# Optimization experiments

Measured on AMD Instinct MI355X. Metric: run time of the kernel, lower is better.

The kernel has to match this reference:

```python
import jax, jax.numpy as jnp
import numpy as np

H = 16            # num heads (sharded)
NOPE = 128        # qk_nope_head_dim
ROPE = 64         # qk_rope_head_dim
VD = 128          # v_head_dim
KV_RANK = 512
HEAD = NOPE + ROPE  # 192
SCALE = HEAD ** (-0.5)  # mscale == 1 (no yarn scaling)
EPS = 1e-6


def rmsnorm(x, w):
    var = jnp.mean(x * x, axis=-1, keepdims=True)
    return x * jax.lax.rsqrt(var + EPS) * w


def apply_rope(pe, cos, sin):
    # pe: [T, h, ROPE]; torch code de-interleaves pairs then applies
    # non-interleaved (rotate-half) rope: out = [e*cos - o*sin, o*cos + e*sin]
    e = pe[..., 0::2]
    o = pe[..., 1::2]
    c = cos[:, None, :]
    s = sin[:, None, :]
    return jnp.concatenate([e * c - o * s, o * c + e * s], axis=-1)


def setup_inputs() -> dict:
    key = jax.random.key(0)
    ks = jax.random.split(key, 10)
    T, D = 4096, 2048
    w = 0.02
    return {
        "hidden_states": jax.random.normal(ks[0], (T, D), jnp.float32),
        "cos": jax.random.uniform(ks[1], (T, ROPE // 2), jnp.float32),
        "sin": jax.random.uniform(ks[2], (T, ROPE // 2), jnp.float32),
        "w_q_a": jax.random.normal(ks[3], (D, 1536), jnp.float32) * w,
        "q_a_ln_w": jnp.ones((1536,), jnp.float32),
        "w_q_b": jax.random.normal(ks[4], (1536, H * HEAD), jnp.float32) * w,
        "w_kv_a": jax.random.normal(ks[5], (D, KV_RANK + ROPE), jnp.float32) * w,
        "kv_a_ln_w": jnp.ones((KV_RANK,), jnp.float32),
        "w_kv_b": jax.random.normal(ks[6], (KV_RANK, H * (NOPE + VD)), jnp.float32) * w,
        "w_o": jax.random.normal(ks[7], (H * VD, D), jnp.float32) * w,
        "batch_size": 2,
    }


def reference(hidden_states, cos, sin, w_q_a, q_a_ln_w, w_q_b, w_kv_a,
              kv_a_ln_w, w_kv_b, w_o, batch_size):
    T, D = hidden_states.shape
    B = int(batch_size)
    S = T // B

    # Q: low-rank down proj -> RMSNorm -> up proj
    q = rmsnorm(hidden_states @ w_q_a, q_a_ln_w) @ w_q_b
    q = q.reshape(T, H, HEAD)
    q_nope = q[..., :NOPE]
    q_pe = apply_rope(q[..., NOPE:], cos, sin)

    # KV: joint down proj with shared rope part (MQA-style)
    ckv = hidden_states @ w_kv_a                        # [T, 512+64]
    compressed_kv = ckv[:, :KV_RANK]
    k_pe = apply_rope(ckv[:, KV_RANK:][:, None, :], cos, sin)  # [T, 1, 64]
    kv = (rmsnorm(compressed_kv, kv_a_ln_w) @ w_kv_b).reshape(T, H, NOPE + VD)
    k_nope = kv[..., :NOPE]
    v = kv[..., NOPE:]                                   # [T, H, 128]

    # Assemble full query/key heads (value pad to 192 + final slice is a no-op
    # mathematically since padded dims are zero; we keep value dim = 128).
    query = jnp.concatenate([q_nope, q_pe], axis=-1)     # [T, H, 192]
    key = jnp.concatenate([k_nope, jnp.broadcast_to(k_pe, (T, H, ROPE))], axis=-1)

    # Causal (prefill) attention per sequence
    qb = query.reshape(B, S, H, HEAD)
    kb = key.reshape(B, S, H, HEAD)
    vb = v.reshape(B, S, H, VD)
    scores = jnp.einsum("bqhd,bkhd->bhqk", qb, kb) * SCALE
    causal = jnp.tril(jnp.ones((S, S), bool))
    scores = jnp.where(causal, scores, jnp.finfo(scores.dtype).min)
    probs = jax.nn.softmax(scores, axis=-1)
    attn = jnp.einsum("bhqk,bkhd->bqhd", probs, vb)      # [B, S, H, 128]

    return attn.reshape(T, H * VD) @ w_o
```

## Files before the change

### kernel.cpp

```cpp
#include <hip/hip_runtime.h>
#include <cstdint>
#include <cstddef>

#define TT 4096
#define DD 2048
#define NH 16
#define HEADD 192
#define NOPE 128
#define VDIM 128
#define SEQ 2048

typedef __bf16 bf16x8 __attribute__((ext_vector_type(8)));
typedef float f32x4 __attribute__((ext_vector_type(4)));
typedef unsigned int u32;

__device__ __forceinline__ float bf2f(unsigned short u) {
    union { unsigned int i; float f; } v; v.i = ((unsigned int)u) << 16; return v.f;
}
__device__ __forceinline__ unsigned short f2bf(float f) {
    union { float f; unsigned int i; } v; v.f = f;
    unsigned int r = v.i + 0x7FFFu + ((v.i >> 16) & 1u);
    return (unsigned short)(r >> 16);
}
__device__ __forceinline__ u32 pack2bf(float a, float b) {
    return (u32)f2bf(a) | ((u32)f2bf(b) << 16);
}
__device__ __forceinline__ void gload16(const unsigned short* g, unsigned short* l) {
    __builtin_amdgcn_global_load_lds((const __attribute__((address_space(1))) u32*)g,
                                     (__attribute__((address_space(3))) u32*)l, 16, 0, 0);
}

#define GMFMA __builtin_amdgcn_mfma_f32_16x16x32_bf16

__global__ __launch_bounds__(256) void cvt_bf16_k(const float* __restrict__ x,
                                                  unsigned short* __restrict__ y, int n) {
    int i = (blockIdx.x * 256 + threadIdx.x) * 4;
    if (i < n) {
        float4 v = *(const float4*)(x + i);
        uint2 o;
        o.x = pack2bf(v.x, v.y);
        o.y = pack2bf(v.z, v.w);
        *(uint2*)(y + i) = o;
    }
}

__global__ __launch_bounds__(256) void transpose_cvt_k(const float* __restrict__ W,
                                                       unsigned short* __restrict__ Wt,
                                                       int K, int N) {
    __shared__ float tile[32][33];
    int n0 = blockIdx.x * 32, k0 = blockIdx.y * 32;
    int t = threadIdx.x, lr = t >> 5, lc = t & 31;
#pragma unroll
    for (int p = 0; p < 4; p++) {
        int k = k0 + lr + p * 8, n = n0 + lc;
        tile[lr + p * 8][lc] = (k < K && n < N) ? W[(size_t)k * N + n] : 0.f;
    }
    __syncthreads();
#pragma unroll
    for (int p = 0; p < 4; p++) {
        int n = n0 + lr + p * 8, k = k0 + lc;
        if (n < N && k < K) Wt[(size_t)n * K + k] = f2bf(tile[lc][lr + p * 8]);
    }
}

template <int BN, typename OT>
__global__ __launch_bounds__(512) void gemm256_k(const unsigned short* __restrict__ A,
                                                 const unsigned short* __restrict__ Bt,
                                                 OT* __restrict__ C,
                                                 int M, int N, int K) {
    constexpr int NREP = BN / 64;
    constexpr int NB = BN / 64;
    constexpr int TILE_E = 8192 + BN * 64;
    __shared__ __align__(16) unsigned short lds[2 * TILE_E];
    const int t = threadIdx.x;
    const int w = t >> 6, lane = t & 63;
    const int wr = w >> 2, wc = w & 3;
    const int l15 = lane & 15, quad = lane >> 4;
    const int bm = blockIdx.y * 128, bn = blockIdx.x * BN;
    const int srow = w * 8 + (lane >> 3);
    const int scol = 8 * ((lane & 7) ^ (lane >> 3));
    const unsigned short* Ag = A + (size_t)(bm + srow) * K + scol;
    const unsigned short* Bg = Bt + (size_t)(bn + srow) * K + scol;
    const int rc0 = (quad * 8) ^ ((l15 & 7) * 8);
    const int rc1 = (32 + quad * 8) ^ ((l15 & 7) * 8);
    f32x4 acc[4][NREP];
    f32x4 zero = {0.f, 0.f, 0.f, 0.f};
#pragma unroll
    for (int i = 0; i < 4; i++)
#pragma unroll
        for (int n = 0; n < NREP; n++) acc[i][n] = zero;
    const int NT = K >> 6;
#pragma unroll
    for (int c = 0; c < 2; c++)
        gload16(Ag + (size_t)c * 64 * K, &lds[c * 4096 + w * 512]);
#pragma unroll
    for (int c = 0; c < NB; c++)
        gload16(Bg + (size_t)c * 64 * K, &lds[8192 + c * 4096 + w * 512]);

    for (int kt = 0; kt < NT; kt++) {
        const int cb = (kt & 1) * TILE_E;
        const int nb = TILE_E - cb;
        const bool more = (kt + 1) < NT;
        asm volatile("s_waitcnt vmcnt(0)" ::: "memory");
        __builtin_amdgcn_s_barrier();
        asm volatile("" ::: "memory");
        const unsigned short* Agk = Ag + (size_t)(kt + 1) * 64;
        const unsigned short* Bgk = Bg + (size_t)(kt + 1) * 64;
        if (more) {
            gload16(Agk, &lds[nb + w * 512]);
            gload16(Agk + (size_t)64 * K, &lds[nb + 4096 + w * 512]);
#pragma unroll
            for (int c = 0; c < NB / 2; c++)
                gload16(Bgk + (size_t)c * 64 * K, &lds[nb + 8192 + c * 4096 + w * 512]);
        }
        bf16x8 a0[2][2], b[NREP][2];
#pragma unroll
        for (int j = 0; j < 2; j++) {
            int rl = wr * 64 + j * 16 + l15;
            a0[j][0] = *(const bf16x8*)&lds[cb + rl * 64 + rc0];
            a0[j][1] = *(const bf16x8*)&lds[cb + rl * 64 + rc1];
        }
#pragma unroll
        for (int n = 0; n < NREP; n++) {
            int rl = wc * (BN / 4) + n * 16 + l15;
            b[n][0] = *(const bf16x8*)&lds[cb + 8192 + rl * 64 + rc0];
            b[n][1] = *(const bf16x8*)&lds[cb + 8192 + rl * 64 + rc1];
        }
        __builtin_amdgcn_s_setprio(1);
#pragma unroll
        for (int j = 0; j < 2; j++)
#pragma unroll
            for (int n = 0; n < NREP; n++) {
                acc[j][n] = GMFMA(a0[j][0], b[n][0], acc[j][n], 0, 0, 0);
                acc[j][n] = GMFMA(a0[j][1], b[n][1], acc[j][n], 0, 0, 0);
            }
        __builtin_amdgcn_s_setprio(0);
        __builtin_amdgcn_s_barrier();
        if (more) {
#pragma unroll
            for (int c = NB / 2; c < NB; c++)
                gload16(Bgk + (size_t)c * 64 * K, &lds[nb + 8192 + c * 4096 + w * 512]);
        }
        bf16x8 a1[2][2];
#pragma unroll
        for (int j = 0; j < 2; j++) {
            int rl = wr * 64 + 32 + j * 16 + l15;
            a1[j][0] = *(const bf16x8*)&lds[cb + rl * 64 + rc0];
            a1[j][1] = *(const bf16x8*)&lds[cb + rl * 64 + rc1];
        }
        __builtin_amdgcn_s_setprio(1);
#pragma unroll
        for (int j = 0; j < 2; j++)
#pragma unroll
            for (int n = 0; n < NREP; n++) {
                acc[2 + j][n] = GMFMA(a1[j][0], b[n][0], acc[2 + j][n], 0, 0, 0);
                acc[2 + j][n] = GMFMA(a1[j][1], b[n][1], acc[2 + j][n], 0, 0, 0);
            }
        __builtin_amdgcn_s_setprio(0);
    }
#pragma unroll
    for (int mi = 0; mi < 4; mi++) {
        int row = bm + wr * 64 + mi * 16 + quad * 4;
#pragma unroll
        for (int n = 0; n < NREP; n++) {
            int col = bn + wc * (BN / 4) + n * 16 + l15;
            OT* cp = C + (size_t)row * N + col;
#pragma unroll
            for (int r = 0; r < 4; r++) {
                float v = acc[mi][n][r];
                if constexpr (sizeof(OT) == 2) cp[(size_t)r * N] = f2bf(v);
                else                            cp[(size_t)r * N] = v;
            }
        }
    }
}

__global__ __launch_bounds__(512) void gemm192_rope_k(const unsigned short* __restrict__ A,
                                                      const unsigned short* __restrict__ Bt,
                                                      const float* __restrict__ cosb,
                                                      const float* __restrict__ sinb,
                                                      unsigned short* __restrict__ Qb) {
    constexpr int K = 1536, N = 3072;
    constexpr int NREP = 3, NB = 3;
    constexpr int TILE_E = 8192 + 192 * 64;
    __shared__ __align__(16) unsigned short lds[2 * TILE_E];
    const int t = threadIdx.x;
    const int w = t >> 6, lane = t & 63;
    const int wr = w >> 2, wc = w & 3;
    const int l15 = lane & 15, quad = lane >> 4;
    const int bm = blockIdx.y * 128, bn = blockIdx.x * 192;
    const int srow = w * 8 + (lane >> 3);
    const int scol = 8 * ((lane & 7) ^ (lane >> 3));
    const unsigned short* Ag = A + (size_t)(bm + srow) * K + scol;
    const unsigned short* Bg = Bt + (size_t)(bn + srow) * K + scol;
    const int rc0 = (quad * 8) ^ ((l15 & 7) * 8);
    const int rc1 = (32 + quad * 8) ^ ((l15 & 7) * 8);
    f32x4 acc[4][NREP];
    f32x4 zero = {0.f, 0.f, 0.f, 0.f};
#pragma unroll
    for (int i = 0; i < 4; i++)
#pragma unroll
        for (int n = 0; n < NREP; n++) acc[i][n] = zero;
    const int NT = K >> 6;
#pragma unroll
    for (int c = 0; c < 2; c++)
        gload16(Ag + (size_t)c * 64 * K, &lds[c * 4096 + w * 512]);
#pragma unroll
    for (int c = 0; c < NB; c++)
        gload16(Bg + (size_t)c * 64 * K, &lds[8192 + c * 4096 + w * 512]);

    for (int kt = 0; kt < NT; kt++) {
        const int cb = (kt & 1) * TILE_E;
        const int nb = TILE_E - cb;
        const bool more = (kt + 1) < NT;
        asm volatile("s_waitcnt vmcnt(0)" ::: "memory");
        __builtin_amdgcn_s_barrier();
        asm volatile("" ::: "memory");
        const unsigned short* Agk = Ag + (size_t)(kt + 1) * 64;
        const unsigned short* Bgk = Bg + (size_t)(kt + 1) * 64;
        if (more) {
            gload16(Agk, &lds[nb + w * 512]);
            gload16(Agk + (size_t)64 * K, &lds[nb + 4096 + w * 512]);
            gload16(Bgk, &lds[nb + 8192 + w * 512]);
        }
        bf16x8 a0[2][2], b[NREP][2];
#pragma unroll
        for (int j = 0; j < 2; j++) {
            int rl = wr * 64 + j * 16 + l15;
            a0[j][0] = *(const bf16x8*)&lds[cb + rl * 64 + rc0];
            a0[j][1] = *(const bf16x8*)&lds[cb + rl * 64 + rc1];
        }
#pragma unroll
        for (int n = 0; n < NREP; n++) {
            int rl = wc * 48 + n * 16 + l15;
            b[n][0] = *(const bf16x8*)&lds[cb + 8192 + rl * 64 + rc0];
            b[n][1] = *(const bf16x8*)&lds[cb + 8192 + rl * 64 + rc1];
        }
        __builtin_amdgcn_s_setprio(1);
#pragma unroll
        for (int j = 0; j < 2; j++)
#pragma unroll
            for (int n = 0; n < NREP; n++) {
                acc[j][n] = GMFMA(a0[j][0], b[n][0], acc[j][n], 0, 0, 0);
                acc[j][n] = GMFMA(a0[j][1], b[n][1], acc[j][n], 0, 0, 0);
            }
        __builtin_amdgcn_s_setprio(0);
        __builtin_amdgcn_s_barrier();
        if (more) {
#pragma unroll
            for (int c = 1; c < NB; c++)
                gload16(Bgk + (size_t)c * 64 * K, &lds[nb + 8192 + c * 4096 + w * 512]);
        }
        bf16x8 a1[2][2];
#pragma unroll
        for (int j = 0; j < 2; j++) {
            int rl = wr * 64 + 32 + j * 16 + l15;
            a1[j][0] = *(const bf16x8*)&lds[cb + rl * 64 + rc0];
            a1[j][1] = *(const bf16x8*)&lds[cb + rl * 64 + rc1];
        }
        __builtin_amdgcn_s_setprio(1);
#pragma unroll
        for (int j = 0; j < 2; j++)
#pragma unroll
            for (int n = 0; n < NREP; n++) {
                acc[2 + j][n] = GMFMA(a1[j][0], b[n][0], acc[2 + j][n], 0, 0, 0);
                acc[2 + j][n] = GMFMA(a1[j][1], b[n][1], acc[2 + j][n], 0, 0, 0);
            }
        __builtin_amdgcn_s_setprio(0);
    }
    __syncthreads();
    unsigned short* Ct = lds;
#pragma unroll
    for (int mi = 0; mi < 4; mi++) {
        int rl = wr * 64 + mi * 16 + quad * 4;
#pragma unroll
        for (int n = 0; n < NREP; n++) {
            int cl = wc * 48 + n * 16 + l15;
#pragma unroll
            for (int r = 0; r < 4; r++)
                Ct[(rl + r) * 200 + cl] = f2bf(acc[mi][n][r]);
        }
    }
    __syncthreads();
    {
        int r = t >> 2, cg = t & 3;
        int trow = bm + r;
        int h = blockIdx.x;
        const float* cr = cosb + (size_t)trow * 32;
        const float* sn = sinb + (size_t)trow * 32;
        unsigned short* dst = Qb + ((size_t)trow * NH + h) * HEADD + cg * 48;
        __align__(16) unsigned short tmp[48];
        const unsigned short* rowp = &Ct[r * 200];
        if (cg < 2) {
#pragma unroll
            for (int i = 0; i < 48; i++) tmp[i] = rowp[cg * 48 + i];
        } else if (cg == 2) {
#pragma unroll
            for (int i = 0; i < 32; i++) tmp[i] = rowp[96 + i];
            const unsigned short* pe = rowp + 128;
#pragma unroll
            for (int jj = 0; jj < 16; jj++) {
                float e = bf2f(pe[2 * jj]), o = bf2f(pe[2 * jj + 1]);
                tmp[32 + jj] = f2bf(e * cr[jj] - o * sn[jj]);
            }
        } else {
            const unsigned short* pe = rowp + 128;
#pragma unroll
            for (int jj = 16; jj < 32; jj++) {
                float e = bf2f(pe[2 * jj]), o = bf2f(pe[2 * jj + 1]);
                tmp[jj - 16] = f2bf(e * cr[jj] - o * sn[jj]);
            }
#pragma unroll
            for (int jj = 0; jj < 32; jj++) {
                float e = bf2f(pe[2 * jj]), o = bf2f(pe[2 * jj + 1]);
                tmp[16 + jj] = f2bf(o * cr[jj] + e * sn[jj]);
            }
        }
#pragma unroll
        for (int g = 0; g < 6; g++)
            *(uint4*)(dst + g * 8) = *(const uint4*)(&tmp[g * 8]);
    }
}

#define KS_STRIDE 200
#define VT_STRIDE 72
#define CS_STRIDE 132

__global__ __launch_bounds__(256) void gemm_kv_k(const unsigned short* __restrict__ A,
                                                 const unsigned short* __restrict__ Bt,
                                                 const unsigned short* __restrict__ kpe,
                                                 unsigned short* __restrict__ Kb2,
                                                 unsigned short* __restrict__ Vt2) {
    const int K = 512;
    __shared__ __align__(16) unsigned short smem[128 * CS_STRIDE];
    unsigned short* As = smem;
    unsigned short* Bs = smem + 128 * 32;
    unsigned short* Cs = smem;
    int bm = blockIdx.y * 128, bn = blockIdx.x * 128;
    int t = threadIdx.x;
    int wave = t >> 6, lane = t & 63;
    int wr = (wave >> 1) * 64, wc = (wave & 1) * 64;
    int l15 = lane & 15, quad = lane >> 4;
    f32x4 acc[4][4];
    f32x4 zero = {0.f, 0.f, 0.f, 0.f};
#pragma unroll
    for (int i = 0; i < 4; i++)
#pragma unroll
        for (int j = 0; j < 4; j++) acc[i][j] = zero;
    int r0 = 16 * (2 * wave) + (lane >> 2);
    int cOff = (lane & 3) * 8;
    const unsigned short* gA0 = A + (size_t)(bm + r0) * K + cOff;
    const unsigned short* gA1 = A + (size_t)(bm + r0 + 16) * K + cOff;
    const unsigned short* gB0 = Bt + (size_t)(bn + r0) * K + cOff;
    const unsigned short* gB1 = Bt + (size_t)(bn + r0 + 16) * K + cOff;
    unsigned short* lA0 = &As[(2 * wave) * 512];
    unsigned short* lA1 = &As[(2 * wave + 1) * 512];
    unsigned short* lB0 = &Bs[(2 * wave) * 512];
    unsigned short* lB1 = &Bs[(2 * wave + 1) * 512];
    for (int k0 = 0; k0 < K; k0 += 32) {
        gload16(gA0 + k0, lA0);
        gload16(gA1 + k0, lA1);
        gload16(gB0 + k0, lB0);
        gload16(gB1 + k0, lB1);
        __syncthreads();
        bf16x8 af[4], bfr[4];
#pragma unroll
        for (int i = 0; i < 4; i++)
            af[i] = *(const bf16x8*)&As[(wr + i * 16 + l15) * 32 + quad * 8];
#pragma unroll
        for (int j = 0; j < 4; j++)
            bfr[j] = *(const bf16x8*)&Bs[(wc + j * 16 + l15) * 32 + quad * 8];
#pragma unroll
        for (int i = 0; i < 4; i++)
#pragma unroll
            for (int j = 0; j < 4; j++)
                acc[i][j] = GMFMA(af[i], bfr[j], acc[i][j], 0, 0, 0);
        __syncthreads();
    }
#pragma unroll
    for (int i = 0; i < 4; i++) {
        int lr = wr + i * 16 + quad * 4;
#pragma unroll
        for (int j = 0; j < 4; j++) {
            int lc = wc + j * 16 + l15;
#pragma unroll
            for (int r = 0; r < 4; r++)
                Cs[(lr + r) * CS_STRIDE + lc] = f2bf(acc[i][j][r]);
        }
    }
    __syncthreads();
    int hh = bn >> 8;
    bool isV = (bn & 255) != 0;
    if (!isV) {
        int row = t >> 1, halfc = t & 1;
        int gs = bm + row;
        int b2 = gs >> 11, s2 = gs & 2047;
        unsigned short* dpb = Kb2 +
            ((size_t)((b2 * NH + hh) * 32 + (s2 >> 6)) * 64 + (s2 & 63)) * KS_STRIDE;
        const unsigned short* sp = &Cs[row * CS_STRIDE + halfc * 64];
        unsigned short* dp = dpb + halfc * 64;
#pragma unroll
        for (int g = 0; g < 8; g++)
            *(uint4*)(dp + g * 8) = *(const uint4*)(sp + g * 8);
        if (halfc) {
            const unsigned short* kp = kpe + (size_t)gs * 64;
            unsigned short* dq = dpb + 128;
#pragma unroll
            for (int g = 0; g < 8; g++)
                *(uint4*)(dq + g * 8) = *(const uint4*)(kp + g * 8);
        }
    } else {
        int kth = t >> 7, dim = t & 127;
        int gs0 = bm + kth * 64;
        int b2 = gs0 >> 11, s20 = gs0 & 2047;
        unsigned short* dp = Vt2 +
            ((size_t)((b2 * NH + hh) * 32 + (s20 >> 6)) * 128 + dim) * VT_STRIDE;
#pragma unroll
        for (int g = 0; g < 8; g++) {
            uint4 o;
            unsigned short* op = (unsigned short*)&o;
#pragma unroll
            for (int q2 = 0; q2 < 8; q2++)
                op[q2] = Cs[(kth * 64 + g * 8 + q2) * CS_STRIDE + dim];
            *(uint4*)(dp + g * 8) = o;
        }
    }
}

__global__ __launch_bounds__(256) void norms_k(const unsigned short* __restrict__ qab,
                                               const float* __restrict__ qw,
                                               const float* __restrict__ kw,
                                               const float* __restrict__ cosb,
                                               const float* __restrict__ sinb,
                                               unsigned short* __restrict__ qan,
                                               unsigned short* __restrict__ ckvn,
                                               unsigned short* __restrict__ kpe) {
    const float QSCALE = 0.07216878364870323f;
    int row = blockIdx.x, t = threadIdx.x;
    const unsigned short* xr = qab + (size_t)row * 2304;
    float s1 = 0.f, s2 = 0.f;
    for (int i = t; i < 1536; i += 256) { float v = bf2f(xr[i]); s1 += v * v; }
#pragma unroll
    for (int i = t; i < 512; i += 256) { float v = bf2f(xr[1536 + i]); s2 += v * v; }
    __shared__ float r1[256], r2[256];
    r1[t] = s1; r2[t] = s2; __syncthreads();
    for (int o = 128; o > 0; o >>= 1) {
        if (t < o) { r1[t] += r1[t + o]; r2[t] += r2[t + o]; }
        __syncthreads();
    }
    float sc1 = rsqrtf(r1[0] / 1536.f + 1e-6f) * QSCALE;
    float sc2 = rsqrtf(r2[0] / 512.f + 1e-6f);
    unsigned short* y1 = qan + (size_t)row * 1536;
    for (int i = t; i < 1536; i += 256) y1[i] = f2bf(bf2f(xr[i]) * sc1 * qw[i]);
    unsigned short* y2 = ckvn + (size_t)row * 512;
#pragma unroll
    for (int i = t; i < 512; i += 256) y2[i] = f2bf(bf2f(xr[1536 + i]) * sc2 * kw[i]);
    if (t < 32) {
        float e = bf2f(xr[2048 + 2 * t]), o = bf2f(xr[2048 + 2 * t + 1]);
        float c = cosb[row * 32 + t], sn = sinb[row * 32 + t];
        kpe[row * 64 + t]      = f2bf(e * c - o * sn);
        kpe[row * 64 + 32 + t] = f2bf(o * c + e * sn);
    }
}

__global__ __launch_bounds__(512) void attn_mfma_k(const unsigned short* __restrict__ Qb,
                                                   const unsigned short* __restrict__ Kb2,
                                                   const unsigned short* __restrict__ Vt2,
                                                   unsigned short* __restrict__ Opart,
                                                   float* __restrict__ Mbuf,
                                                   float* __restrict__ Lbuf) {
    __shared__ __align__(16) unsigned short Ks[64 * KS_STRIDE];
    __shared__ __align__(16) unsigned short Vts[128 * VT_STRIDE];
    int xe = 39 - blockIdx.x;
    int h  = blockIdx.y;
    int b  = blockIdx.z;
    int qt = 0, accn = 0;
    while (true) { int c = (qt >> 2) + 1; if (xe < accn + c) break; accn += c; qt++; }
    int chunk = xe - accn;
    int t = threadIdx.x;
    int w = t >> 6, lane = t & 63;
    int l15 = lane & 15, quad = lane >> 4;
    int bh = b * NH + h;
    int q0 = b * SEQ + qt * 128;
    int qglob = qt * 128 + w * 16 + l15;
    int flat = bh * 40 + xe;

    bf16x8 qf[6];
    {
        const unsigned short* qbase = Qb + ((size_t)(q0 + w * 16 + l15) * NH + h) * HEADD + quad * 8;
#pragma unroll
        for (int c = 0; c < 6; c++)
            qf[c] = *(const bf16x8*)(qbase + c * 32);
    }
    f32x4 acc_o[8];
    f32x4 zero = {0.f, 0.f, 0.f, 0.f};
#pragma unroll
    for (int j = 0; j < 8; j++) acc_o[j] = zero;
    float mrun = -1e30f, lrun = 0.f;

    int kt0 = chunk * 8, kt1 = min(kt0 + 7, 2 * qt + 1);
    int cbeg = w * 5 + min(w, 3), cnt = (w < 3) ? 6 : 5;
    for (int kt = kt0; kt <= kt1; kt++) {
        __syncthreads();
        {
            const unsigned short* kg = Kb2 + ((size_t)bh * 32 + kt) * (64 * KS_STRIDE) + lane * 8;
            const unsigned short* vg = Vt2 + ((size_t)bh * 32 + kt) * (128 * VT_STRIDE) + lane * 8;
            for (int c = cbeg; c < cbeg + cnt; c++) {
                if (c < 25) gload16(kg + c * 512, &Ks[c * 512]);
                else        gload16(vg + (c - 25) * 512, &Vts[(c - 25) * 512]);
            }
        }
        __syncthreads();
        f32x4 acc_s[4];
#pragma unroll
        for (int j = 0; j < 4; j++) acc_s[j] = zero;
#pragma unroll
        for (int c = 0; c < 6; c++) {
#pragma unroll
            for (int j = 0; j < 4; j++) {
                bf16x8 kf = *(const bf16x8*)&Ks[(j * 16 + l15) * KS_STRIDE + c * 32 + quad * 8];
                acc_s[j] = GMFMA(kf, qf[c], acc_s[j], 0, 0, 0);
            }
        }
        float sv[4][4];
        const bool needmask = (kt * 64 + 63) > (qt * 128 + w * 16);
        if (needmask) {
#pragma unroll
            for (int j = 0; j < 4; j++) {
                int kbase = kt * 64 + j * 16 + quad * 4;
#pragma unroll
                for (int r = 0; r < 4; r++)
                    sv[j][r] = (kbase + r > qglob) ? -1e30f : acc_s[j][r];
            }
        } else {
#pragma unroll
            for (int j = 0; j < 4; j++)
#pragma unroll
                for (int r = 0; r < 4; r++) sv[j][r] = acc_s[j][r];
        }
        float v = sv[0][0];
#pragma unroll
        for (int j = 0; j < 4; j++)
#pragma unroll
            for (int r = 0; r < 4; r++) v = fmaxf(v, sv[j][r]);
        v = fmaxf(v, __shfl_xor(v, 16));
        v = fmaxf(v, __shfl_xor(v, 32));
        if (!__all(v - mrun <= 8.f)) {
            float mnew = fmaxf(mrun, v);
            float alpha = __expf(mrun - mnew);
            mrun = mnew;
            lrun *= alpha;
#pragma unroll
            for (int jt = 0; jt < 8; jt++)
#pragma unroll
                for (int r = 0; r < 4; r++) acc_o[jt][r] *= alpha;
        }
        float rs = 0.f;
#pragma unroll
        for (int j = 0; j < 4; j++)
#pragma unroll
            for (int r = 0; r < 4; r++) { float p = __expf(sv[j][r] - mrun); sv[j][r] = p; rs += p; }
        rs += __shfl_xor(rs, 16);
        rs += __shfl_xor(rs, 32);
        lrun += rs;
        u32 pk[4][2];
#pragma unroll
        for (int j = 0; j < 4; j++) {
            pk[j][0] = pack2bf(sv[j][0], sv[j][1]);
            pk[j][1] = pack2bf(sv[j][2], sv[j][3]);
        }
        int laneA = (((2 * quad) & 3) << 4) + l15;
        int laneB = (((2 * quad + 1) & 3) << 4) + l15;
        bool hi = (quad & 2) != 0;
#pragma unroll
        for (int c2 = 0; c2 < 2; c2++) {
            u32 a0 = __shfl(pk[2 * c2][0], laneA),     a1 = __shfl(pk[2 * c2][1], laneA);
            u32 b0 = __shfl(pk[2 * c2 + 1][0], laneA), b1 = __shfl(pk[2 * c2 + 1][1], laneA);
            u32 a2 = __shfl(pk[2 * c2][0], laneB),     a3 = __shfl(pk[2 * c2][1], laneB);
            u32 b2 = __shfl(pk[2 * c2 + 1][0], laneB), b3 = __shfl(pk[2 * c2 + 1][1], laneB);
            union { u32 d[4]; bf16x8 v8; } pf;
            pf.d[0] = hi ? b0 : a0;
            pf.d[1] = hi ? b1 : a1;
            pf.d[2] = hi ? b2 : a2;
            pf.d[3] = hi ? b3 : a3;
#pragma unroll
            for (int jt = 0; jt < 8; jt++) {
                bf16x8 vf = *(const bf16x8*)&Vts[(jt * 16 + l15) * VT_STRIDE + c2 * 32 + quad * 8];
                acc_o[jt] = GMFMA(vf, pf.v8, acc_o[jt], 0, 0, 0);
            }
        }
    }
    {
        int row = w * 16 + l15;
        unsigned short* op = Opart + (size_t)flat * 16384 + row * 128;
#pragma unroll
        for (int jt = 0; jt < 8; jt++) {
            uint2 o;
            o.x = pack2bf(acc_o[jt][0], acc_o[jt][1]);
            o.y = pack2bf(acc_o[jt][2], acc_o[jt][3]);
            *(uint2*)(op + jt * 16 + quad * 4) = o;
        }
        if (quad == 0) {
            Mbuf[(size_t)flat * 128 + row] = mrun;
            Lbuf[(size_t)flat * 128 + row] = lrun;
        }
    }
}

__global__ __launch_bounds__(256) void attn_combine_k(const unsigned short* __restrict__ Opart,
                                                      const float* __restrict__ Mbuf,
                                                      const float* __restrict__ Lbuf,
                                                      unsigned short* __restrict__ attnb) {
    int q64 = blockIdx.x, h = blockIdx.y, b = blockIdx.z;
    int qt = q64 >> 1, half = q64 & 1;
    int nch = (qt >> 2) + 1;
    int F = 0;
    for (int q = 0; q < qt; q++) F += (q >> 2) + 1;
    int flat0 = (b * NH + h) * 40 + F;
    int t = threadIdx.x;
    int row = t >> 2, d0 = (t & 3) * 32;
    int row128 = half * 64 + row;
    float mc[4], lc[4], wgt[4];
    float mstar = -1e30f;
#pragma unroll
    for (int c = 0; c < 4; c++) {
        if (c < nch) {
            mc[c] = Mbuf[(size_t)(flat0 + c) * 128 + row128];
            lc[c] = Lbuf[(size_t)(flat0 + c) * 128 + row128];
        } else { mc[c] = -1e30f; lc[c] = 0.f; }
        mstar = fmaxf(mstar, mc[c]);
    }
    float L = 0.f;
#pragma unroll
    for (int c = 0; c < 4; c++) { wgt[c] = __expf(mc[c] - mstar); L += wgt[c] * lc[c]; }
    float invL = 1.f / L;
    float acc[32];
#pragma unroll
    for (int j = 0; j < 32; j++) acc[j] = 0.f;
#pragma unroll
    for (int c = 0; c < 4; c++) {
        if (c < nch) {
            const unsigned short* src = Opart + (size_t)(flat0 + c) * 16384 + row128 * 128 + d0;
            float wc = wgt[c];
#pragma unroll
            for (int g = 0; g < 4; g++) {
                uint4 u = *(const uint4*)(src + g * 8);
                const unsigned short* sp = (const unsigned short*)&u;
#pragma unroll
                for (int j = 0; j < 8; j++) acc[g * 8 + j] += wc * bf2f(sp[j]);
            }
        }
    }
    unsigned short* dst = attnb + (size_t)(b * SEQ + q64 * 64 + row) * 2048 + h * 128 + d0;
#pragma unroll
    for (int g = 0; g < 4; g++) {
        uint4 o;
        unsigned short* sp = (unsigned short*)&o;
#pragma unroll
        for (int j = 0; j < 8; j++) sp[j] = f2bf(acc[g * 8 + j] * invL);
        *(uint4*)(dst + g * 8) = o;
    }
}

extern "C" void kernel_launch(void* const* d_in, const int* in_sizes, int n_in,
                              void* d_out, int out_size, void* d_ws, size_t ws_size,
                              hipStream_t stream) {
    const float* hs     = (const float*)d_in[0];
    const float* cosb   = (const float*)d_in[1];
    const float* sinb   = (const float*)d_in[2];
    const float* w_q_a  = (const float*)d_in[3];
    const float* q_ln   = (const float*)d_in[4];
    const float* w_q_b  = (const float*)d_in[5];
    const float* w_kv_a = (const float*)d_in[6];
    const float* kv_ln  = (const float*)d_in[7];
    const float* w_kv_b = (const float*)d_in[8];
    const float* w_o    = (const float*)d_in[9];
    float* out = (float*)d_out;

    char* base = (char*)d_ws;
    size_t off = 0;
    auto take = [&](size_t bytes) { void* p = base + off; off += (bytes + 255) & ~(size_t)255; return p; };
    unsigned short* wqabT = (unsigned short*)take((size_t)2304 * 2048 * 2);
    unsigned short* wqbT  = (unsigned short*)take((size_t)3072 * 1536 * 2);
    unsigned short* wkvbT = (unsigned short*)take((size_t)4096 * 512 * 2);
    unsigned short* woT   = (unsigned short*)take((size_t)2048 * 2048 * 2);
    unsigned short* hsb   = (unsigned short*)take((size_t)TT * DD * 2);
    unsigned short* qab   = (unsigned short*)take((size_t)TT * 2304 * 2);
    unsigned short* qan   = (unsigned short*)take((size_t)TT * 1536 * 2);
    unsigned short* ckvn  = (unsigned short*)take((size_t)TT * 512 * 2);
    unsigned short* kpe   = (unsigned short*)take((size_t)TT * 64 * 2);
    unsigned short* Qbuf  = (unsigned short*)take((size_t)TT * NH * HEADD * 2);
    unsigned short* Kb2   = (unsigned short*)take((size_t)32 * 32 * 64 * KS_STRIDE * 2);
    unsigned short* Vt2   = (unsigned short*)take((size_t)32 * 32 * 128 * VT_STRIDE * 2);
    unsigned short* attnb = (unsigned short*)take((size_t)TT * 2048 * 2);
    unsigned short* Opart = (unsigned short*)take((size_t)1280 * 16384 * 2);
    float* Mbuf = (float*)take((size_t)1280 * 128 * 4);
    float* Lbuf = (float*)take((size_t)1280 * 128 * 4);

    cvt_bf16_k<<<(TT * DD) / 1024, 256, 0, stream>>>(hs, hsb, TT * DD);
    transpose_cvt_k<<<dim3(1536 / 32, 2048 / 32), 256, 0, stream>>>(w_q_a, wqabT, 2048, 1536);
    transpose_cvt_k<<<dim3(18, 2048 / 32), 256, 0, stream>>>(w_kv_a, wqabT + (size_t)1536 * 2048, 2048, 576);
    transpose_cvt_k<<<dim3(3072 / 32, 1536 / 32), 256, 0, stream>>>(w_q_b, wqbT, 1536, 3072);
    transpose_cvt_k<<<dim3(4096 / 32, 512 / 32), 256, 0, stream>>>(w_kv_b, wkvbT, 512, 4096);
    transpose_cvt_k<<<dim3(2048 / 32, 2048 / 32), 256, 0, stream>>>(w_o, woT, 2048, 2048);

    gemm256_k<128, unsigned short><<<dim3(18, 32), 512, 0, stream>>>(hsb, wqabT, qab, 4096, 2304, 2048);
    norms_k<<<4096, 256, 0, stream>>>(qab, q_ln, kv_ln, cosb, sinb, qan, ckvn, kpe);
    gemm192_rope_k<<<dim3(16, 32), 512, 0, stream>>>(qan, wqbT, cosb, sinb, Qbuf);
    gemm_kv_k<<<dim3(32, 32), 256, 0, stream>>>(ckvn, wkvbT, kpe, Kb2, Vt2);
    attn_mfma_k<<<dim3(40, 16, 2), 512, 0, stream>>>(Qbuf, Kb2, Vt2, Opart, Mbuf, Lbuf);
    attn_combine_k<<<dim3(32, 16, 2), 256, 0, stream>>>(Opart, Mbuf, Lbuf, attnb);
    gemm256_k<128, float><<<dim3(16, 32), 512, 0, stream>>>(attnb, woT, out, 4096, 2048, 2048);
}
```

Baseline: 498.9 us.

## Replace 128x128 GEMM with 128x256 triple-buffered four-phase pipelined GEMM

The generic bf16 GEMM used for the fused Q/KV down-projection and the output projection is replaced by a 128x256 tile kernel. It uses three LDS buffers with a two-tile-ahead prefetch, and each k-step is split into four compute phases that interleave staging loads for k+2 with MFMA work, waiting on partial vmcnt. The larger tile halves the grid and raises data reuse per block. In exchange it uses much more LDS (144 KB), leaves fewer blocks to fill the CUs, and adds more barriers per k-step.

Result: slower. 535.4 us (+7.3%).

```diff
diff --git a/kernel.cpp b/kernel.cpp
--- a/kernel.cpp
+++ b/kernel.cpp
@@ -63,111 +63,112 @@
     }
 }
 
-template <int BN, typename OT>
-__global__ __launch_bounds__(512) void gemm256_k(const unsigned short* __restrict__ A,
-                                                 const unsigned short* __restrict__ Bt,
-                                                 OT* __restrict__ C,
-                                                 int M, int N, int K) {
-    constexpr int NREP = BN / 64;
-    constexpr int NB = BN / 64;
-    constexpr int TILE_E = 8192 + BN * 64;
-    __shared__ __align__(16) unsigned short lds[2 * TILE_E];
+template <typename OT>
+__global__ __launch_bounds__(512) void gemm8p_k(const unsigned short* __restrict__ A,
+                                                const unsigned short* __restrict__ Bt,
+                                                OT* __restrict__ C,
+                                                int M, int N, int K) {
+    constexpr int TILE_E = 24576;
+    __shared__ __align__(16) unsigned short lds[3 * TILE_E];
     const int t = threadIdx.x;
     const int w = t >> 6, lane = t & 63;
     const int wr = w >> 2, wc = w & 3;
     const int l15 = lane & 15, quad = lane >> 4;
-    const int bm = blockIdx.y * 128, bn = blockIdx.x * BN;
+    const int bm = blockIdx.y * 128, bn = blockIdx.x * 256;
     const int srow = w * 8 + (lane >> 3);
     const int scol = 8 * ((lane & 7) ^ (lane >> 3));
     const unsigned short* Ag = A + (size_t)(bm + srow) * K + scol;
     const unsigned short* Bg = Bt + (size_t)(bn + srow) * K + scol;
-    const int rc0 = (quad * 8) ^ ((l15 & 7) * 8);
-    const int rc1 = (32 + quad * 8) ^ ((l15 & 7) * 8);
-    f32x4 acc[4][NREP];
+    const int rca0 = 8 * (quad ^ (l15 & 7));
+    const int rca1 = 8 * ((4 + quad) ^ (l15 & 7));
+    f32x4 acc[4][4];
     f32x4 zero = {0.f, 0.f, 0.f, 0.f};
 #pragma unroll
     for (int i = 0; i < 4; i++)
 #pragma unroll
-        for (int n = 0; n < NREP; n++) acc[i][n] = zero;
+        for (int j = 0; j < 4; j++) acc[i][j] = zero;
     const int NT = K >> 6;
-#pragma unroll
-    for (int c = 0; c < 2; c++)
-        gload16(Ag + (size_t)c * 64 * K, &lds[c * 4096 + w * 512]);
-#pragma unroll
-    for (int c = 0; c < NB; c++)
-        gload16(Bg + (size_t)c * 64 * K, &lds[8192 + c * 4096 + w * 512]);
-
-    for (int kt = 0; kt < NT; kt++) {
-        const int cb = (kt & 1) * TILE_E;
-        const int nb = TILE_E - cb;
-        const bool more = (kt + 1) < NT;
-        asm volatile("s_waitcnt vmcnt(0)" ::: "memory");
+
+    auto stage_unit = [&](int kt, int u, unsigned short* dst) {
+        unsigned short* lb = dst + (u == 0 ? 0 : 8192 + (u - 1) * 8192);
+        const unsigned short* gb =
+            (u == 0 ? Ag : Bg + (size_t)(u - 1) * 128 * K) + (size_t)kt * 64;
+        gload16(gb, lb + w * 512);
+        gload16(gb + (size_t)64 * K, lb + 4096 + w * 512);
+    };
+
+    auto phase = [&](unsigned short* cb, int qd, bool dostage, int kst, int ust,
+                     unsigned short* sb, bool dogate, bool vm6) {
+        const int mg = qd >> 1, ng = qd & 1;
+        bf16x8 a_[2][2], b_[2][2];
+#pragma unroll
+        for (int x = 0; x < 2; x++) {
+            int rl = wr * 64 + (mg * 2 + x) * 16 + l15;
+            a_[x][0] = *(const bf16x8*)&cb[rl * 64 + rca0];
+            a_[x][1] = *(const bf16x8*)&cb[rl * 64 + rca1];
+            int cl = wc * 64 + (ng * 2 + x) * 16 + l15;
+            b_[x][0] = *(const bf16x8*)&cb[8192 + cl * 64 + rca0];
+            b_[x][1] = *(const bf16x8*)&cb[8192 + cl * 64 + rca1];
+        }
+        if (dostage) stage_unit(kst, ust, sb);
+        asm volatile("" ::: "memory");
         __builtin_amdgcn_s_barrier();
         asm volatile("" ::: "memory");
-        const unsigned short* Agk = Ag + (size_t)(kt + 1) * 64;
-        const unsigned short* Bgk = Bg + (size_t)(kt + 1) * 64;
-        if (more) {
-            gload16(Agk, &lds[nb + w * 512]);
-            gload16(Agk + (size_t)64 * K, &lds[nb + 4096 + w * 512]);
-#pragma unroll
-            for (int c = 0; c < NB / 2; c++)
-                gload16(Bgk + (size_t)c * 64 * K, &lds[nb + 8192 + c * 4096 + w * 512]);
-        }
-        bf16x8 a0[2][2], b[NREP][2];
-#pragma unroll
-        for (int j = 0; j < 2; j++) {
-            int rl = wr * 64 + j * 16 + l15;
-            a0[j][0] = *(const bf16x8*)&lds[cb + rl * 64 + rc0];
-            a0[j][1] = *(const bf16x8*)&lds[cb + rl * 64 + rc1];
-        }
-#pragma unroll
-        for (int n = 0; n < NREP; n++) {
-            int rl = wc * (BN / 4) + n * 16 + l15;
-            b[n][0] = *(const bf16x8*)&lds[cb + 8192 + rl * 64 + rc0];
-            b[n][1] = *(const bf16x8*)&lds[cb + 8192 + rl * 64 + rc1];
-        }
         __builtin_amdgcn_s_setprio(1);
 #pragma unroll
-        for (int j = 0; j < 2; j++)
-#pragma unroll
-            for (int n = 0; n < NREP; n++) {
-                acc[j][n] = GMFMA(a0[j][0], b[n][0], acc[j][n], 0, 0, 0);
-                acc[j][n] = GMFMA(a0[j][1], b[n][1], acc[j][n], 0, 0, 0);
+        for (int x = 0; x < 2; x++)
+#pragma unroll
+            for (int y = 0; y < 2; y++) {
+                acc[mg * 2 + x][ng * 2 + y] =
+                    GMFMA(a_[x][0], b_[y][0], acc[mg * 2 + x][ng * 2 + y], 0, 0, 0);
+                acc[mg * 2 + x][ng * 2 + y] =
+                    GMFMA(a_[x][1], b_[y][1], acc[mg * 2 + x][ng * 2 + y], 0, 0, 0);
             }
         __builtin_amdgcn_s_setprio(0);
+        if (dogate) {
+            if (vm6) asm volatile("s_waitcnt vmcnt(6)" ::: "memory");
+            else     asm volatile("s_waitcnt vmcnt(0)" ::: "memory");
+        }
+        asm volatile("" ::: "memory");
         __builtin_amdgcn_s_barrier();
-        if (more) {
-#pragma unroll
-            for (int c = NB / 2; c < NB; c++)
-                gload16(Bgk + (size_t)c * 64 * K, &lds[nb + 8192 + c * 4096 + w * 512]);
-        }
-        bf16x8 a1[2][2];
-#pragma unroll
-        for (int j = 0; j < 2; j++) {
-            int rl = wr * 64 + 32 + j * 16 + l15;
-            a1[j][0] = *(const bf16x8*)&lds[cb + rl * 64 + rc0];
-            a1[j][1] = *(const bf16x8*)&lds[cb + rl * 64 + rc1];
-        }
-        __builtin_amdgcn_s_setprio(1);
-#pragma unroll
-        for (int j = 0; j < 2; j++)
-#pragma unroll
-            for (int n = 0; n < NREP; n++) {
-                acc[2 + j][n] = GMFMA(a1[j][0], b[n][0], acc[2 + j][n], 0, 0, 0);
-                acc[2 + j][n] = GMFMA(a1[j][1], b[n][1], acc[2 + j][n], 0, 0, 0);
-            }
-        __builtin_amdgcn_s_setprio(0);
+        asm volatile("" ::: "memory");
+    };
+
+    {
+        unsigned short* d0 = &lds[0];
+        unsigned short* d1 = &lds[TILE_E];
+#pragma unroll
+        for (int u = 0; u < 3; u++) stage_unit(0, u, d0);
+#pragma unroll
+        for (int u = 0; u < 3; u++) stage_unit(1, u, d1);
+        asm volatile("s_waitcnt vmcnt(6)" ::: "memory");
+        asm volatile("" ::: "memory");
+        __builtin_amdgcn_s_barrier();
+        asm volatile("" ::: "memory");
+    }
+    int cur = 0, nx2 = 2;
+    for (int g = 0; g < NT; g++) {
+        unsigned short* cb = &lds[cur * TILE_E];
+        unsigned short* sb = &lds[nx2 * TILE_E];
+        const bool st = (g + 2) < NT;
+        const bool lastg = (g + 1) == NT;
+        phase(cb, 0, st, g + 2, 0, sb, false, false);
+        phase(cb, 1, st, g + 2, 1, sb, false, false);
+        phase(cb, 2, st, g + 2, 2, sb, false, false);
+        phase(cb, 3, false, 0, 0, sb, !lastg, st);
+        cur = (cur + 1 == 3) ? 0 : cur + 1;
+        nx2 = (nx2 + 1 == 3) ? 0 : nx2 + 1;
     }
 #pragma unroll
     for (int mi = 0; mi < 4; mi++) {
         int row = bm + wr * 64 + mi * 16 + quad * 4;
 #pragma unroll
-        for (int n = 0; n < NREP; n++) {
-            int col = bn + wc * (BN / 4) + n * 16 + l15;
+        for (int ni = 0; ni < 4; ni++) {
+            int col = bn + wc * 64 + ni * 16 + l15;
             OT* cp = C + (size_t)row * N + col;
 #pragma unroll
             for (int r = 0; r < 4; r++) {
-                float v = acc[mi][n][r];
+                float v = acc[mi][ni][r];
                 if constexpr (sizeof(OT) == 2) cp[(size_t)r * N] = f2bf(v);
                 else                            cp[(size_t)r * N] = v;
             }
@@ -704,11 +705,11 @@
     transpose_cvt_k<<<dim3(4096 / 32, 512 / 32), 256, 0, stream>>>(w_kv_b, wkvbT, 512, 4096);
     transpose_cvt_k<<<dim3(2048 / 32, 2048 / 32), 256, 0, stream>>>(w_o, woT, 2048, 2048);
 
-    gemm256_k<128, unsigned short><<<dim3(18, 32), 512, 0, stream>>>(hsb, wqabT, qab, 4096, 2304, 2048);
+    gemm8p_k<unsigned short><<<dim3(9, 32), 512, 0, stream>>>(hsb, wqabT, qab, 4096, 2304, 2048);
     norms_k<<<4096, 256, 0, stream>>>(qab, q_ln, kv_ln, cosb, sinb, qan, ckvn, kpe);
     gemm192_rope_k<<<dim3(16, 32), 512, 0, stream>>>(qan, wqbT, cosb, sinb, Qbuf);
     gemm_kv_k<<<dim3(32, 32), 256, 0, stream>>>(ckvn, wkvbT, kpe, Kb2, Vt2);
     attn_mfma_k<<<dim3(40, 16, 2), 512, 0, stream>>>(Qbuf, Kb2, Vt2, Opart, Mbuf, Lbuf);
     attn_combine_k<<<dim3(32, 16, 2), 256, 0, stream>>>(Opart, Mbuf, Lbuf, attnb);
-    gemm256_k<128, float><<<dim3(16, 32), 512, 0, stream>>>(attnb, woT, out, 4096, 2048, 2048);
-}
+    gemm8p_k<float><<<dim3(8, 32), 512, 0, stream>>>(attnb, woT, out, 4096, 2048, 2048);
+}
```
